# Optimization experiments

Measured on AMD Instinct MI355X. Metric: run time of the kernel, lower is better.

The kernel has to match this reference:

```python
import jax, jax.numpy as jnp
import numpy as np

MI, DIS, DIN, HID, L, H, NG, H1, OUT = 2048, 1024, 3072, 256, 15, 8, 8, 512, 64
DENOM = 4.0 / 7.0  # (grid_max - grid_min) / (num_grids - 1)
EPS = 1e-5


def _ln(x, g, b):
    m = jnp.mean(x, axis=-1, keepdims=True)
    v = jnp.mean((x - m) ** 2, axis=-1, keepdims=True)
    return (x - m) * jax.lax.rsqrt(v + EPS) * g + b


def _fastkan(x, ln_g, ln_b, grid, Ws, Wb, bb):
    xn = _ln(x, ln_g, ln_b)
    basis = jnp.exp(-(((xn[..., None] - grid) / DENOM) ** 2))  # [N, DIN, NG]
    ret = basis.reshape(x.shape[0], -1) @ Ws.T                  # SplineLinear (no bias)
    return ret + jax.nn.silu(x) @ Wb.T + bb                      # base update


def _hgcn(x, G, W, attn, bias, rW1, rb1, rW2, rb2, ln_g, ln_b, jk_W, jk_b):
    # per-layer multi-head conv: mean_h a_h * G @ (x @ W_h) == G @ (x @ (sum_h a_h W_h / H))
    def step(xc, p):
        W_l, a_l, b_l, rW1_l, rb1_l, rW2_l, rb2_l, g_l, be_l = p
        W_eff = jnp.einsum('h,hio->io', a_l, W_l) / H
        out = G @ (xc @ W_eff) + b_l
        gate = jax.nn.sigmoid(jax.nn.relu(out @ rW1_l.T + rb1_l) @ rW2_l.T + rb2_l)
        out = _ln(out * gate, g_l, be_l)
        out = jnp.where(out >= 0, out, 0.25 * out)  # leaky_relu(0.25); dropout off (eval)
        return out, out
    _, outs = jax.lax.scan(step, x, (W, attn, bias, rW1, rb1, rW2, rb2, ln_g, ln_b))
    jk = jnp.moveaxis(outs, 0, 1).reshape(x.shape[0], L * HID)   # jumping-knowledge concat
    return jk @ jk_W.T + jk_b


def _mlp3(x, W1, b1, W2, b2, W3, b3):
    h = jax.nn.relu(x @ W1.T + b1)
    h = jax.nn.relu(h @ W2.T + b2)
    return jax.nn.relu(h @ W3.T + b3)


def _forward(concat_mi, concat_dis, G_mi, G_dis, AT, A, rbf_grid, mi_kan_ln_g, mi_kan_ln_b, mi_kan_Ws, mi_kan_Wb, mi_kan_bb, dis_kan_ln_g, dis_kan_ln_b, dis_kan_Ws, dis_kan_Wb, dis_kan_bb, mi_W, mi_attn, mi_bias, mi_rW1, mi_rb1, mi_rW2, mi_rb2, mi_ln_g, mi_ln_b, mi_jk_W, mi_jk_b, dis_W, dis_attn, dis_bias, dis_rW1, dis_rb1, dis_rW2, dis_rb2, dis_ln_g, dis_ln_b, dis_jk_W, dis_jk_b, lx_W1, lx_b1, lx_W2, lx_b2, lx_W3, lx_b3, ly_W1, ly_b1, ly_W2, ly_b2, ly_W3, ly_b3, ne_W, ne_b, he_W, he_b, mun_W, mun_b, mue_W, mue_b):
    # AT and A are accepted by the original forward but never used in its body.
    mi_e = _fastkan(concat_mi, mi_kan_ln_g, mi_kan_ln_b, rbf_grid, mi_kan_Ws, mi_kan_Wb, mi_kan_bb)
    dis_e = _fastkan(concat_dis, dis_kan_ln_g, dis_kan_ln_b, rbf_grid, dis_kan_Ws, dis_kan_Wb, dis_kan_bb)
    mi_f = _hgcn(mi_e, G_mi, mi_W, mi_attn, mi_bias, mi_rW1, mi_rb1, mi_rW2, mi_rb2, mi_ln_g, mi_ln_b, mi_jk_W, mi_jk_b)
    dis_f = _hgcn(dis_e, G_dis, dis_W, dis_attn, dis_bias, dis_rW1, dis_rb1, dis_rW2, dis_rb2, dis_ln_g, dis_ln_b, dis_jk_W, dis_jk_b)
    x = _mlp3(mi_f, lx_W1, lx_b1, lx_W2, lx_b2, lx_W3, lx_b3)
    y = _mlp3(dis_f, ly_W1, ly_b1, ly_W2, ly_b2, ly_W3, ly_b3)
    result_h = x @ y.T                                           # [MI, DIS]
    z_node = jax.nn.relu(concat_mi @ ne_W.T + ne_b)              # node_encoders1 (eval: no dropout)
    z_edge = jax.nn.relu(concat_dis @ he_W.T + he_b)             # hyperedge_encoders1
    z_node_mean = z_node @ mun_W.T + mun_b                       # _enc_mu_node (identity act)
    z_edge_mean = z_edge @ mue_W.T + mue_b                       # _enc_mu_hedge
    recon = z_node_mean @ z_edge_mean.T                          # decoder2 with identity act
    score = 0.7 * jax.nn.sigmoid(recon) + 0.3 * jax.nn.sigmoid(result_h)
    return score, recon


def setup_inputs() -> dict:
    ks = iter(jax.random.split(jax.random.key(0), 96))
    nrm = lambda shape, s: jax.random.normal(next(ks), shape, dtype=jnp.float32) * s
    uni = lambda shape: jax.random.uniform(next(ks), shape, dtype=jnp.float32)
    d = {}
    d['concat_mi'] = nrm((MI, DIN), 1.0)
    d['concat_dis'] = nrm((DIS, DIN), 1.0)
    d['G_mi'] = uni((MI, MI)) / MI    # row-normalized dense hypergraph adjacency
    d['G_dis'] = uni((DIS, DIS)) / DIS
    d['AT'] = uni((DIS, MI))
    d['A'] = uni((MI, DIS))
    d['rbf_grid'] = jnp.linspace(-2.0, 2.0, NG).astype(jnp.float32)
    for p in ('mi', 'dis'):
        d[p + '_kan_ln_g'] = jnp.ones((DIN,), jnp.float32)
        d[p + '_kan_ln_b'] = jnp.zeros((DIN,), jnp.float32)
        d[p + '_kan_Ws'] = nrm((HID, DIN * NG), 0.02)
        d[p + '_kan_Wb'] = nrm((HID, DIN), 0.02)
        d[p + '_kan_bb'] = nrm((HID,), 0.01)
        d[p + '_W'] = nrm((L, H, HID, HID), 0.06)
        d[p + '_attn'] = jnp.ones((L, H), jnp.float32)
        d[p + '_bias'] = nrm((L, HID), 0.01)
        d[p + '_rW1'] = nrm((L, HID // 4, HID), 0.05)
        d[p + '_rb1'] = nrm((L, HID // 4), 0.01)
        d[p + '_rW2'] = nrm((L, HID, HID // 4), 0.05)
        d[p + '_rb2'] = nrm((L, HID), 0.01)
        d[p + '_ln_g'] = jnp.ones((L, HID), jnp.float32)
        d[p + '_ln_b'] = jnp.zeros((L, HID), jnp.float32)
        d[p + '_jk_W'] = nrm((HID, L * HID), 0.02)
        d[p + '_jk_b'] = nrm((HID,), 0.01)
    for p in ('lx', 'ly'):
        d[p + '_W1'] = nrm((256, HID), 0.05); d[p + '_b1'] = nrm((256,), 0.01)
        d[p + '_W2'] = nrm((128, 256), 0.05); d[p + '_b2'] = nrm((128,), 0.01)
        d[p + '_W3'] = nrm((64, 128), 0.05); d[p + '_b3'] = nrm((64,), 0.01)
    d['ne_W'] = nrm((H1, DIN), 0.02); d['ne_b'] = nrm((H1,), 0.01)
    d['he_W'] = nrm((H1, DIN), 0.02); d['he_b'] = nrm((H1,), 0.01)
    d['mun_W'] = nrm((OUT, H1), 0.02); d['mun_b'] = nrm((OUT,), 0.01)
    d['mue_W'] = nrm((OUT, H1), 0.02); d['mue_b'] = nrm((OUT,), 0.01)
    return d


def reference(concat_mi, concat_dis, G_mi, G_dis, AT, A, rbf_grid, mi_kan_ln_g, mi_kan_ln_b, mi_kan_Ws, mi_kan_Wb, mi_kan_bb, dis_kan_ln_g, dis_kan_ln_b, dis_kan_Ws, dis_kan_Wb, dis_kan_bb, mi_W, mi_attn, mi_bias, mi_rW1, mi_rb1, mi_rW2, mi_rb2, mi_ln_g, mi_ln_b, mi_jk_W, mi_jk_b, dis_W, dis_attn, dis_bias, dis_rW1, dis_rb1, dis_rW2, dis_rb2, dis_ln_g, dis_ln_b, dis_jk_W, dis_jk_b, lx_W1, lx_b1, lx_W2, lx_b2, lx_W3, lx_b3, ly_W1, ly_b1, ly_W2, ly_b2, ly_W3, ly_b3, ne_W, ne_b, he_W, he_b, mun_W, mun_b, mue_W, mue_b):
    return _forward(concat_mi, concat_dis, G_mi, G_dis, AT, A, rbf_grid, mi_kan_ln_g, mi_kan_ln_b, mi_kan_Ws, mi_kan_Wb, mi_kan_bb, dis_kan_ln_g, dis_kan_ln_b, dis_kan_Ws, dis_kan_Wb, dis_kan_bb, mi_W, mi_attn, mi_bias, mi_rW1, mi_rb1, mi_rW2, mi_rb2, mi_ln_g, mi_ln_b, mi_jk_W, mi_jk_b, dis_W, dis_attn, dis_bias, dis_rW1, dis_rb1, dis_rW2, dis_rb2, dis_ln_g, dis_ln_b, dis_jk_W, dis_jk_b, lx_W1, lx_b1, lx_W2, lx_b2, lx_W3, lx_b3, ly_W1, ly_b1, ly_W2, ly_b2, ly_W3, ly_b3, ne_W, ne_b, he_W, he_b, mun_W, mun_b, mue_W, mue_b)
```

## Files before the change

kernel.cpp:

```cpp
#include <hip/hip_runtime.h>
#include <cstdint>
#include <cstddef>

typedef unsigned short u16;
typedef __attribute__((ext_vector_type(8))) short short8;
typedef __attribute__((ext_vector_type(4))) float f32x4;

#define MI_N  2048
#define DIS_N 1024
#define TOT_N 3072
#define DIN   3072
#define HID   256
#define LL    15
#define NG    8

__device__ __forceinline__ float b2f(u16 u) {
  unsigned int v = ((unsigned int)u) << 16;
  float f;
  __builtin_memcpy(&f, &v, 4);
  return f;
}
__device__ __forceinline__ u16 f2b(float f) {
  unsigned int u;
  __builtin_memcpy(&u, &f, 4);
  u = (u + 0x7fffu + ((u >> 16) & 1u)) >> 16;
  return (u16)u;
}
__device__ __forceinline__ float sigf(float x) { return 1.f / (1.f + __expf(-x)); }

#define NSEG 20
struct CvtJobs {
  const float* src[NSEG];
  u16* dst[NSEG];
  int nblk[NSEG];
  int nseg;
};

__global__ __launch_bounds__(256) void cvt_f2b(CvtJobs j) {
  int b = blockIdx.x, s = 0;
  while (s + 1 < j.nseg && b >= j.nblk[s]) { b -= j.nblk[s]; ++s; }
  const long base = ((long)b * 256 + threadIdx.x) * 8;
  const float4 v0 = *(const float4*)(j.src[s] + base);
  const float4 v1 = *(const float4*)(j.src[s] + base + 4);
  short8 o;
  o[0] = (short)f2b(v0.x); o[1] = (short)f2b(v0.y);
  o[2] = (short)f2b(v0.z); o[3] = (short)f2b(v0.w);
  o[4] = (short)f2b(v1.x); o[5] = (short)f2b(v1.y);
  o[6] = (short)f2b(v1.z); o[7] = (short)f2b(v1.w);
  *(short8*)(j.dst[s] + base) = o;
}

struct GP {
  const u16* A; int lda;
  const u16* B; int ldb;
  void* C; int ldc;
  const float* bias;
  int K;
  int mblk;
};

template <int ACT, int TRANS, int F32OUT, int NCT>
__global__ __launch_bounds__(64) void gemm_bt(GP p0, GP p1) {
  GP p = p0;
  int bx = blockIdx.x;
  if (bx >= p0.mblk) { bx -= p0.mblk; p = p1; }
  const int lane = threadIdx.x;
  const int m16 = lane & 15, quad = lane >> 4;
  const int kph = quad * 8;
  const long row0 = (long)bx * 32 + m16;
  const long colBase = (long)blockIdx.y * (16 * NCT);
  f32x4 acc[2][NCT] = {};
  const u16* A0 = p.A + row0 * (long)p.lda + kph;
  const u16* A1 = A0 + 16L * p.lda;
  const u16* Bb = p.B + (colBase + m16) * (long)p.ldb + kph;
  const long bstep = 16L * p.ldb;
  for (int kk = 0; kk < p.K; kk += 32) {
    short8 a0 = *(const short8*)(A0 + kk);
    short8 a1 = *(const short8*)(A1 + kk);
#pragma unroll
    for (int c = 0; c < NCT; ++c) {
      short8 b = *(const short8*)(Bb + c * bstep + kk);
      acc[0][c] = __builtin_amdgcn_mfma_f32_16x16x32_bf16(a0, b, acc[0][c], 0, 0, 0);
      acc[1][c] = __builtin_amdgcn_mfma_f32_16x16x32_bf16(a1, b, acc[1][c], 0, 0, 0);
    }
  }
#pragma unroll
  for (int c = 0; c < NCT; ++c) {
    const long col = colBase + c * 16 + m16;
    const float bv = p.bias ? p.bias[col] : 0.f;
#pragma unroll
    for (int r = 0; r < 2; ++r) {
      const long orow = (long)bx * 32 + r * 16 + quad * 4;
#pragma unroll
      for (int j = 0; j < 4; ++j) {
        float v = acc[r][c][j] + bv;
        if (ACT == 1) v = fmaxf(v, 0.f);
        if (ACT == 2) v = sigf(v);
        if (F32OUT)
          ((float*)p.C)[(orow + j) * (long)p.ldc + col] = v;
        else if (TRANS)
          ((u16*)p.C)[col * (long)p.ldc + orow + j] = f2b(v);
        else
          ((u16*)p.C)[(orow + j) * (long)p.ldc + col] = f2b(v);
      }
    }
  }
}

struct FKP {
  const u16* xn; const u16* xb;
  const u16* Ws; const u16* Wb;
  float* partial;
  int rowoff;
  int mblk;
};

__global__ __launch_bounds__(64) void fastkan_gemm(FKP p0, FKP p1, const float* grid8) {
  FKP p = p0;
  int bx = blockIdx.x;
  if (bx >= p0.mblk) { bx -= p0.mblk; p = p1; }
  const int chunk = blockIdx.z;
  const int lane = threadIdx.x;
  const int m16 = lane & 15, quad = lane >> 4, kph = quad * 8;
  const long row0 = (long)bx * 32 + m16;
  const long colBase = (long)blockIdx.y * 128;
  f32x4 acc[2][8] = {};
  if (chunk < 4) {
    float gv[8];
#pragma unroll
    for (int j = 0; j < 8; ++j) gv[j] = grid8[j];
    const u16* xn0 = p.xn + row0 * (long)DIN;
    const u16* xn1 = xn0 + 16L * DIN;
    const int k0 = chunk * 6144, k1 = k0 + 6144;
    for (int kk = k0; kk < k1; kk += 32) {
      const int d = (kk >> 3) + quad;
      const float x0 = b2f(xn0[d]);
      const float x1 = b2f(xn1[d]);
      short8 a0, a1;
#pragma unroll
      for (int j = 0; j < 8; ++j) {
        float t0 = (x0 - gv[j]) * 1.75f;
        float t1 = (x1 - gv[j]) * 1.75f;
        a0[j] = (short)f2b(__expf(-t0 * t0));
        a1[j] = (short)f2b(__expf(-t1 * t1));
      }
#pragma unroll
      for (int c = 0; c < 8; ++c) {
        const u16* Bp = p.Ws + (colBase + c * 16 + m16) * (long)(DIN * NG) + kk + kph;
        short8 b = *(const short8*)Bp;
        acc[0][c] = __builtin_amdgcn_mfma_f32_16x16x32_bf16(a0, b, acc[0][c], 0, 0, 0);
        acc[1][c] = __builtin_amdgcn_mfma_f32_16x16x32_bf16(a1, b, acc[1][c], 0, 0, 0);
      }
    }
  } else {
    const u16* x0p = p.xb + row0 * (long)DIN + kph;
    const u16* x1p = x0p + 16L * DIN;
    for (int kk = 0; kk < DIN; kk += 32) {
      short8 r0 = *(const short8*)(x0p + kk);
      short8 r1 = *(const short8*)(x1p + kk);
      short8 a0, a1;
#pragma unroll
      for (int j = 0; j < 8; ++j) {
        float v0 = b2f((u16)r0[j]);
        float v1 = b2f((u16)r1[j]);
        a0[j] = (short)f2b(v0 * sigf(v0));
        a1[j] = (short)f2b(v1 * sigf(v1));
      }
#pragma unroll
      for (int c = 0; c < 8; ++c) {
        const u16* Bp = p.Wb + (colBase + c * 16 + m16) * (long)DIN + kk + kph;
        short8 b = *(const short8*)Bp;
        acc[0][c] = __builtin_amdgcn_mfma_f32_16x16x32_bf16(a0, b, acc[0][c], 0, 0, 0);
        acc[1][c] = __builtin_amdgcn_mfma_f32_16x16x32_bf16(a1, b, acc[1][c], 0, 0, 0);
      }
    }
  }
  float* outp = p.partial + ((long)chunk * TOT_N + p.rowoff) * HID;
#pragma unroll
  for (int c = 0; c < 8; ++c) {
    const long col = colBase + c * 16 + m16;
#pragma unroll
    for (int r = 0; r < 2; ++r) {
      const long orow = (long)bx * 32 + r * 16 + quad * 4;
#pragma unroll
      for (int j = 0; j < 4; ++j) outp[(orow + j) * HID + col] = acc[r][c][j];
    }
  }
}

__global__ __launch_bounds__(256) void fk_combine(const float* partial, const float* bb_mi,
                                                  const float* bb_dis, u16* e) {
  const long i = (long)blockIdx.x * 256 + threadIdx.x;
  const int c = (int)(i & 255);
  const long n = i >> 8;
  float s = 0.f;
#pragma unroll
  for (int pI = 0; pI < 5; ++pI) s += partial[(long)pI * TOT_N * HID + i];
  s += (n < MI_N ? bb_mi : bb_dis)[c];
  e[i] = f2b(s);
}

__global__ __launch_bounds__(256) void weff_kernel(const float* Wmi, const float* Ami,
                                                   const float* Wdis, const float* Adis,
                                                   u16* outT) {
  const int b = blockIdx.x;
  const int s = b / 3840;
  const int r = b % 3840;
  const int l = r >> 8;
  const int t = r & 255;
  const int i0 = (t >> 4) << 4;
  const int o0 = (t & 15) << 4;
  const float* W = (s ? Wdis : Wmi) + (long)l * 8 * 65536;
  const float* A = (s ? Adis : Ami) + l * 8;
  const int tx = threadIdx.x & 15;
  const int ty = threadIdx.x >> 4;
  float sum = 0.f;
#pragma unroll
  for (int h = 0; h < 8; ++h)
    sum += A[h] * W[(long)h * 65536 + (long)(i0 + ty) * 256 + o0 + tx];
  sum *= 0.125f;
  __shared__ float tile[16][17];
  tile[ty][tx] = sum;
  __syncthreads();
  outT[((long)s * LL + l) * 65536 + (long)(o0 + ty) * 256 + i0 + tx] = f2b(tile[tx][ty]);
}

__device__ __forceinline__ void breduce2(float& a, float& b) {
  for (int o = 32; o > 0; o >>= 1) {
    a += __shfl_down(a, o);
    b += __shfl_down(b, o);
  }
  __shared__ float sm[8];
  const int w = threadIdx.x >> 6;
  const int lane = threadIdx.x & 63;
  if (lane == 0) { sm[w] = a; sm[4 + w] = b; }
  __syncthreads();
  if (threadIdx.x == 0) {
    sm[0] = sm[0] + sm[1] + sm[2] + sm[3];
    sm[4] = sm[4] + sm[5] + sm[6] + sm[7];
  }
  __syncthreads();
  a = sm[0];
  b = sm[4];
}

__global__ __launch_bounds__(256) void ln_silu(const float* xmi, const float* xdis,
                                               const float* gmi, const float* bmi,
                                               const float* gdis, const float* bdis,
                                               u16* xn, u16* cbf) {
  const int n = blockIdx.x;
  const bool ds = (n >= MI_N);
  const float* x = ds ? xdis + (long)(n - MI_N) * DIN : xmi + (long)n * DIN;
  const float* g = ds ? gdis : gmi;
  const float* be = ds ? bdis : bmi;
  float xv[12];
  float s1 = 0.f, s2 = 0.f;
#pragma unroll
  for (int j = 0; j < 12; ++j) {
    xv[j] = x[j * 256 + threadIdx.x];
    s1 += xv[j];
    s2 += xv[j] * xv[j];
  }
  breduce2(s1, s2);
  const float m = s1 * (1.f / DIN);
  const float inv = rsqrtf(s2 * (1.f / DIN) - m * m + 1e-5f);
#pragma unroll
  for (int j = 0; j < 12; ++j) {
    const int e = j * 256 + threadIdx.x;
    xn[(long)n * DIN + e] = f2b((xv[j] - m) * inv * g[e] + be[e]);
    cbf[(long)n * DIN + e] = f2b(xv[j]);
  }
}

__global__ __launch_bounds__(256) void gate_ln(const u16* hout, const u16* gate,
                                               const float* gmi, const float* bmi,
                                               const float* gdis, const float* bdis,
                                               u16* jk, int l) {
  const int n = blockIdx.x;
  const int c = threadIdx.x;
  const bool ds = (n >= MI_N);
  const float* g = (ds ? gdis : gmi) + l * HID;
  const float* be = (ds ? bdis : bmi) + l * HID;
  const float h = b2f(hout[(long)n * HID + c]) * b2f(gate[(long)n * HID + c]);
  float s1 = h, s2 = h * h;
  breduce2(s1, s2);
  const float m = s1 * (1.f / HID);
  const float var = s2 * (1.f / HID) - m * m;
  float y = (h - m) * rsqrtf(var + 1e-5f) * g[c] + be[c];
  y = (y >= 0.f) ? y : 0.25f * y;
  jk[(long)n * (LL * HID) + l * HID + c] = f2b(y);
}

__global__ __launch_bounds__(256) void final_combine(const float* rh, float* out) {
  const long i = (long)blockIdx.x * 256 + threadIdx.x;
  const float rc = out[(long)MI_N * DIS_N + i];
  out[i] = 0.7f * sigf(rc) + 0.3f * sigf(rh[i]);
}

extern "C" void kernel_launch(void* const* d_in, const int* in_sizes, int n_in,
                              void* d_out, int out_size, void* d_ws, size_t ws_size,
                              hipStream_t stream) {
  const float* concat_mi   = (const float*)d_in[0];
  const float* concat_dis  = (const float*)d_in[1];
  const float* G_mi        = (const float*)d_in[2];
  const float* G_dis       = (const float*)d_in[3];
  const float* rbf_grid    = (const float*)d_in[6];
  const float* mi_kan_ln_g = (const float*)d_in[7];
  const float* mi_kan_ln_b = (const float*)d_in[8];
  const float* mi_kan_Ws   = (const float*)d_in[9];
  const float* mi_kan_Wb   = (const float*)d_in[10];
  const float* mi_kan_bb   = (const float*)d_in[11];
  const float* mi_W        = (const float*)d_in[12];
  const float* mi_attn     = (const float*)d_in[13];
  const float* mi_bias     = (const float*)d_in[14];
  const float* mi_rW1      = (const float*)d_in[15];
  const float* mi_rb1      = (const float*)d_in[16];
  const float* mi_rW2      = (const float*)d_in[17];
  const float* mi_rb2      = (const float*)d_in[18];
  const float* mi_ln_g     = (const float*)d_in[19];
  const float* mi_ln_b     = (const float*)d_in[20];
  const float* mi_jk_W     = (const float*)d_in[21];
  const float* mi_jk_b     = (const float*)d_in[22];
  const float* dis_kan_ln_g = (const float*)d_in[23];
  const float* dis_kan_ln_b = (const float*)d_in[24];
  const float* dis_kan_Ws  = (const float*)d_in[25];
  const float* dis_kan_Wb  = (const float*)d_in[26];
  const float* dis_kan_bb  = (const float*)d_in[27];
  const float* dis_W       = (const float*)d_in[28];
  const float* dis_attn    = (const float*)d_in[29];
  const float* dis_bias    = (const float*)d_in[30];
  const float* dis_rW1     = (const float*)d_in[31];
  const float* dis_rb1     = (const float*)d_in[32];
  const float* dis_rW2     = (const float*)d_in[33];
  const float* dis_rb2     = (const float*)d_in[34];
  const float* dis_ln_g    = (const float*)d_in[35];
  const float* dis_ln_b    = (const float*)d_in[36];
  const float* dis_jk_W    = (const float*)d_in[37];
  const float* dis_jk_b    = (const float*)d_in[38];
  const float* lx_W1 = (const float*)d_in[39]; const float* lx_b1 = (const float*)d_in[40];
  const float* lx_W2 = (const float*)d_in[41]; const float* lx_b2 = (const float*)d_in[42];
  const float* lx_W3 = (const float*)d_in[43]; const float* lx_b3 = (const float*)d_in[44];
  const float* ly_W1 = (const float*)d_in[45]; const float* ly_b1 = (const float*)d_in[46];
  const float* ly_W2 = (const float*)d_in[47]; const float* ly_b2 = (const float*)d_in[48];
  const float* ly_W3 = (const float*)d_in[49]; const float* ly_b3 = (const float*)d_in[50];
  const float* ne_W  = (const float*)d_in[51]; const float* ne_b  = (const float*)d_in[52];
  const float* he_W  = (const float*)d_in[53]; const float* he_b  = (const float*)d_in[54];
  const float* mun_W = (const float*)d_in[55]; const float* mun_b = (const float*)d_in[56];
  const float* mue_W = (const float*)d_in[57]; const float* mue_b = (const float*)d_in[58];

  char* wp = (char*)d_ws;
  size_t off = 0;
  auto alloc = [&](size_t bytes) -> void* {
    void* p = wp + off;
    off += (bytes + 255) & ~(size_t)255;
    return p;
  };
  u16* cbf    = (u16*)alloc((size_t)TOT_N * DIN * 2);
  u16* gmib   = (u16*)alloc((size_t)MI_N * MI_N * 2);
  u16* gdisb  = (u16*)alloc((size_t)DIS_N * DIS_N * 2);
  u16* wsb0   = (u16*)alloc((size_t)256 * 24576 * 2);
  u16* wsb1   = (u16*)alloc((size_t)256 * 24576 * 2);
  u16* wbb0   = (u16*)alloc((size_t)256 * 3072 * 2);
  u16* wbb1   = (u16*)alloc((size_t)256 * 3072 * 2);
  u16* jkwb0  = (u16*)alloc((size_t)256 * 3840 * 2);
  u16* jkwb1  = (u16*)alloc((size_t)256 * 3840 * 2);
  u16* rw1b0  = (u16*)alloc((size_t)LL * 64 * 256 * 2);
  u16* rw1b1  = (u16*)alloc((size_t)LL * 64 * 256 * 2);
  u16* rw2b0  = (u16*)alloc((size_t)LL * 256 * 64 * 2);
  u16* rw2b1  = (u16*)alloc((size_t)LL * 256 * 64 * 2);
  u16* lxw1b  = (u16*)alloc((size_t)256 * 256 * 2);
  u16* lxw2b  = (u16*)alloc((size_t)128 * 256 * 2);
  u16* lxw3b  = (u16*)alloc((size_t)64 * 128 * 2);
  u16* lyw1b  = (u16*)alloc((size_t)256 * 256 * 2);
  u16* lyw2b  = (u16*)alloc((size_t)128 * 256 * 2);
  u16* lyw3b  = (u16*)alloc((size_t)64 * 128 * 2);
  u16* neb    = (u16*)alloc((size_t)512 * 3072 * 2);
  u16* heb    = (u16*)alloc((size_t)512 * 3072 * 2);
  u16* munb   = (u16*)alloc((size_t)64 * 512 * 2);
  u16* mueb   = (u16*)alloc((size_t)64 * 512 * 2);
  u16* wefft  = (u16*)alloc((size_t)2 * LL * 65536 * 2);
  u16* e      = (u16*)alloc((size_t)TOT_N * HID * 2);
  u16* t1t    = (u16*)alloc((size_t)HID * TOT_N * 2);
  u16* hout   = (u16*)alloc((size_t)TOT_N * HID * 2);
  u16* g1b    = (u16*)alloc((size_t)TOT_N * 64 * 2);
  u16* gateb  = (u16*)alloc((size_t)TOT_N * HID * 2);
  u16* jk     = (u16*)alloc((size_t)TOT_N * LL * HID * 2);
  u16* fb     = (u16*)alloc((size_t)TOT_N * HID * 2);
  char* regA  = (char*)alloc(35000000);
  u16* xn     = (u16*)regA;
  float* fkp  = (float*)(regA + 18874624);
  u16* h1b    = (u16*)regA;
  u16* h2b    = (u16*)(regA + 1572864);
  u16* xyb    = (u16*)(regA + 2359296);
  float* rh   = (float*)(regA + 2752512);
  u16* zb     = (u16*)(regA + 11141120);
  u16* zm     = (u16*)(regA + 14286848);
  float* outf = (float*)d_out;
  float* rec  = outf + (size_t)MI_N * DIS_N;
  (void)ws_size; (void)in_sizes; (void)n_in; (void)out_size;

  const dim3 B64(64), B256(256);

  {
    CvtJobs cj{};
    int ns = 0, total = 0;
    auto push = [&](const float* s, u16* dst, int count) {
      cj.src[ns] = s; cj.dst[ns] = dst; cj.nblk[ns] = count / 2048;
      total += count / 2048; ++ns;
    };
    push(G_mi, gmib, MI_N * MI_N);
    push(G_dis, gdisb, DIS_N * DIS_N);
    push(mi_kan_Ws, wsb0, 256 * 24576);
    push(dis_kan_Ws, wsb1, 256 * 24576);
    push(mi_kan_Wb, wbb0, 256 * 3072);
    push(dis_kan_Wb, wbb1, 256 * 3072);
    push(mi_jk_W, jkwb0, 256 * 3840);
    push(dis_jk_W, jkwb1, 256 * 3840);
    push(mi_rW1, rw1b0, LL * 64 * 256);
    push(dis_rW1, rw1b1, LL * 64 * 256);
    push(mi_rW2, rw2b0, LL * 256 * 64);
    push(dis_rW2, rw2b1, LL * 256 * 64);
    push(lx_W1, lxw1b, 256 * 256);
    push(lx_W2, lxw2b, 128 * 256);
    push(lx_W3, lxw3b, 64 * 128);
    push(ly_W1, lyw1b, 256 * 256);
    push(ly_W2, lyw2b, 128 * 256);
    push(ly_W3, lyw3b, 64 * 128);
    push(ne_W, neb, 512 * 3072);
    push(he_W, heb, 512 * 3072);
    cj.nseg = ns;
    cvt_f2b<<<dim3(total), B256, 0, stream>>>(cj);
    CvtJobs cj2{};
    cj2.src[0] = mun_W; cj2.dst[0] = munb; cj2.nblk[0] = (64 * 512) / 2048;
    cj2.src[1] = mue_W; cj2.dst[1] = mueb; cj2.nblk[1] = (64 * 512) / 2048;
    cj2.nseg = 2;
    cvt_f2b<<<dim3(32), B256, 0, stream>>>(cj2);
  }
  ln_silu<<<dim3(TOT_N), B256, 0, stream>>>(concat_mi, concat_dis, mi_kan_ln_g, mi_kan_ln_b,
                                            dis_kan_ln_g, dis_kan_ln_b, xn, cbf);
  weff_kernel<<<dim3(2 * LL * 256), B256, 0, stream>>>(mi_W, mi_attn, dis_W, dis_attn, wefft);
  {
    FKP f0{xn, cbf, wsb0, wbb0, fkp, 0, 64};
    FKP f1{xn + (size_t)MI_N * DIN, cbf + (size_t)MI_N * DIN, wsb1, wbb1, fkp, MI_N, 32};
    fastkan_gemm<<<dim3(96, 2, 5), B64, 0, stream>>>(f0, f1, rbf_grid);
    fk_combine<<<dim3(TOT_N * HID / 256), B256, 0, stream>>>(fkp, mi_kan_bb, dis_kan_bb, e);
  }
  for (int l = 0; l < LL; ++l) {
    const u16* xc0 = (l == 0) ? e : jk + (size_t)(l - 1) * HID;
    const u16* xc1 = (l == 0) ? e + (size_t)MI_N * HID
                              : jk + (size_t)MI_N * LL * HID + (size_t)(l - 1) * HID;
    const int xlda = (l == 0) ? HID : LL * HID;
    GP a0{xc0, xlda, wefft + (size_t)l * 65536, 256, t1t, MI_N, nullptr, 256, 64};
    GP a1{xc1, xlda, wefft + ((size_t)LL + l) * 65536, 256, t1t + (size_t)HID * MI_N, DIS_N,
          nullptr, 256, 32};
    gemm_bt<0, 1, 0, 4><<<dim3(96, 4), B64, 0, stream>>>(a0, a1);
    GP h0{gmib, MI_N, t1t, MI_N, hout, HID, mi_bias + l * HID, MI_N, 64};
    GP h1{gdisb, DIS_N, t1t + (size_t)HID * MI_N, DIS_N, hout + (size_t)MI_N * HID, HID,
          dis_bias + l * HID, DIS_N, 32};
    gemm_bt<0, 0, 0, 4><<<dim3(96, 4), B64, 0, stream>>>(h0, h1);
    GP g0{hout, HID, rw1b0 + (size_t)l * 64 * HID, HID, g1b, 64, mi_rb1 + l * 64, HID, 64};
    GP g1{hout + (size_t)MI_N * HID, HID, rw1b1 + (size_t)l * 64 * HID, HID,
          g1b + (size_t)MI_N * 64, 64, dis_rb1 + l * 64, HID, 32};
    gemm_bt<1, 0, 0, 4><<<dim3(96, 1), B64, 0, stream>>>(g0, g1);
    GP s0{g1b, 64, rw2b0 + (size_t)l * HID * 64, 64, gateb, HID, mi_rb2 + l * HID, 64, 64};
    GP s1{g1b + (size_t)MI_N * 64, 64, rw2b1 + (size_t)l * HID * 64, 64,
          gateb + (size_t)MI_N * HID, HID, dis_rb2 + l * HID, 64, 32};
    gemm_bt<2, 0, 0, 4><<<dim3(96, 4), B64, 0, stream>>>(s0, s1);
    gate_ln<<<dim3(TOT_N), B256, 0, stream>>>(hout, gateb, mi_ln_g, mi_ln_b, dis_ln_g,
                                              dis_ln_b, jk, l);
  }
  {
    GP j0{jk, LL * HID, jkwb0, LL * HID, fb, HID, mi_jk_b, LL * HID, 64};
    GP j1{jk + (size_t)MI_N * LL * HID, LL * HID, jkwb1, LL * HID, fb + (size_t)MI_N * HID,
          HID, dis_jk_b, LL * HID, 32};
    gemm_bt<0, 0, 0, 4><<<dim3(96, 4), B64, 0, stream>>>(j0, j1);
  }
  {
    GP m0{fb, HID, lxw1b, HID, h1b, 256, lx_b1, HID, 64};
    GP m1{fb + (size_t)MI_N * HID, HID, lyw1b, HID, h1b + (size_t)MI_N * 256, 256, ly_b1,
          HID, 32};
    gemm_bt<1, 0, 0, 4><<<dim3(96, 4), B64, 0, stream>>>(m0, m1);
    GP n0{h1b, 256, lxw2b, 256, h2b, 128, lx_b2, 256, 64};
    GP n1{h1b + (size_t)MI_N * 256, 256, lyw2b, 256, h2b + (size_t)MI_N * 128, 128, ly_b2,
          256, 32};
    gemm_bt<1, 0, 0, 4><<<dim3(96, 2), B64, 0, stream>>>(n0, n1);
    GP o0{h2b, 128, lxw3b, 128, xyb, 64, lx_b3, 128, 64};
    GP o1{h2b + (size_t)MI_N * 128, 128, lyw3b, 128, xyb + (size_t)MI_N * 64, 64, ly_b3,
          128, 32};
    gemm_bt<1, 0, 0, 4><<<dim3(96, 1), B64, 0, stream>>>(o0, o1);
  }
  {
    GP r0{xyb, 64, xyb + (size_t)MI_N * 64, 64, rh, DIS_N, nullptr, 64, 64};
    gemm_bt<0, 0, 1, 4><<<dim3(64, 16), B64, 0, stream>>>(r0, r0);
  }
  {
    GP e0{cbf, DIN, neb, DIN, zb, 512, ne_b, DIN, 64};
    GP e1{cbf + (size_t)MI_N * DIN, DIN, heb, DIN, zb + (size_t)MI_N * 512, 512, he_b, DIN,
          32};
    gemm_bt<1, 0, 0, 4><<<dim3(96, 8), B64, 0, stream>>>(e0, e1);
  }
  {
    GP u0{zb, 512, munb, 512, zm, 64, mun_b, 512, 64};
    GP u1{zb + (size_t)MI_N * 512, 512, mueb, 512, zm + (size_t)MI_N * 64, 64, mue_b, 512,
          32};
    gemm_bt<0, 0, 0, 4><<<dim3(96, 1), B64, 0, stream>>>(u0, u1);
  }
  {
    GP c0{zm, 64, zm + (size_t)MI_N * 64, 64, rec, DIS_N, nullptr, 64, 64};
    gemm_bt<0, 0, 1, 4><<<dim3(64, 16), B64, 0, stream>>>(c0, c0);
  }
  final_combine<<<dim3(MI_N * DIS_N / 256), B256, 0, stream>>>(rh, outf);
}
```

Before: 1.690 ms.

## Split GEMM K-loop across four waves with LDS reduction

Both the generic GEMM kernel and the fastkan GEMM now launch 256 threads (four wavefronts) per block instead of 64. Each wave handles every fourth 32-wide K slice, and the partial accumulators are combined through shared memory in a two-step tree before wave 0 writes the result. The aim is more waves in flight on the small grids (96x4 blocks), which should better hide memory latency. In exchange it adds LDS traffic, barriers and register pressure. For small K (64) two waves get no slices and only contribute zeros.

```diff
diff --git a/kernel.cpp b/kernel.cpp
--- a/kernel.cpp
+++ b/kernel.cpp
@@ -60,11 +60,13 @@
 };
 
 template <int ACT, int TRANS, int F32OUT, int NCT>
-__global__ __launch_bounds__(64) void gemm_bt(GP p0, GP p1) {
+__global__ __launch_bounds__(256) void gemm_bt(GP p0, GP p1) {
   GP p = p0;
   int bx = blockIdx.x;
   if (bx >= p0.mblk) { bx -= p0.mblk; p = p1; }
-  const int lane = threadIdx.x;
+  const int tid = threadIdx.x;
+  const int w = tid >> 6;
+  const int lane = tid & 63;
   const int m16 = lane & 15, quad = lane >> 4;
   const int kph = quad * 8;
   const long row0 = (long)bx * 32 + m16;
@@ -74,7 +76,7 @@
   const u16* A1 = A0 + 16L * p.lda;
   const u16* Bb = p.B + (colBase + m16) * (long)p.ldb + kph;
   const long bstep = 16L * p.ldb;
-  for (int kk = 0; kk < p.K; kk += 32) {
+  for (int kk = w * 32; kk < p.K; kk += 128) {
     short8 a0 = *(const short8*)(A0 + kk);
     short8 a1 = *(const short8*)(A1 + kk);
 #pragma unroll
@@ -84,6 +86,26 @@
       acc[1][c] = __builtin_amdgcn_mfma_f32_16x16x32_bf16(a1, b, acc[1][c], 0, 0, 0);
     }
   }
+  __shared__ float red[2][64][NCT * 8 + 1];
+  float* av = (float*)acc;
+  if (w >= 2) {
+#pragma unroll
+    for (int i = 0; i < NCT * 8; ++i) red[w - 2][lane][i] = av[i];
+  }
+  __syncthreads();
+  if (w < 2) {
+#pragma unroll
+    for (int i = 0; i < NCT * 8; ++i) av[i] += red[w][lane][i];
+  }
+  __syncthreads();
+  if (w == 1) {
+#pragma unroll
+    for (int i = 0; i < NCT * 8; ++i) red[0][lane][i] = av[i];
+  }
+  __syncthreads();
+  if (w != 0) return;
+#pragma unroll
+  for (int i = 0; i < NCT * 8; ++i) av[i] += red[0][lane][i];
 #pragma unroll
   for (int c = 0; c < NCT; ++c) {
     const long col = colBase + c * 16 + m16;
@@ -115,12 +137,14 @@
   int mblk;
 };
 
-__global__ __launch_bounds__(64) void fastkan_gemm(FKP p0, FKP p1, const float* grid8) {
+__global__ __launch_bounds__(256) void fastkan_gemm(FKP p0, FKP p1, const float* grid8) {
   FKP p = p0;
   int bx = blockIdx.x;
   if (bx >= p0.mblk) { bx -= p0.mblk; p = p1; }
   const int chunk = blockIdx.z;
-  const int lane = threadIdx.x;
+  const int tid = threadIdx.x;
+  const int w = tid >> 6;
+  const int lane = tid & 63;
   const int m16 = lane & 15, quad = lane >> 4, kph = quad * 8;
   const long row0 = (long)bx * 32 + m16;
   const long colBase = (long)blockIdx.y * 128;
@@ -132,7 +156,7 @@
     const u16* xn0 = p.xn + row0 * (long)DIN;
     const u16* xn1 = xn0 + 16L * DIN;
     const int k0 = chunk * 6144, k1 = k0 + 6144;
-    for (int kk = k0; kk < k1; kk += 32) {
+    for (int kk = k0 + w * 32; kk < k1; kk += 128) {
       const int d = (kk >> 3) + quad;
       const float x0 = b2f(xn0[d]);
       const float x1 = b2f(xn1[d]);
@@ -155,7 +179,7 @@
   } else {
     const u16* x0p = p.xb + row0 * (long)DIN + kph;
     const u16* x1p = x0p + 16L * DIN;
-    for (int kk = 0; kk < DIN; kk += 32) {
+    for (int kk = w * 32; kk < DIN; kk += 128) {
       short8 r0 = *(const short8*)(x0p + kk);
       short8 r1 = *(const short8*)(x1p + kk);
       short8 a0, a1;
@@ -175,6 +199,26 @@
       }
     }
   }
+  __shared__ float red[2][64][65];
+  float* av = (float*)acc;
+  if (w >= 2) {
+#pragma unroll
+    for (int i = 0; i < 64; ++i) red[w - 2][lane][i] = av[i];
+  }
+  __syncthreads();
+  if (w < 2) {
+#pragma unroll
+    for (int i = 0; i < 64; ++i) av[i] += red[w][lane][i];
+  }
+  __syncthreads();
+  if (w == 1) {
+#pragma unroll
+    for (int i = 0; i < 64; ++i) red[0][lane][i] = av[i];
+  }
+  __syncthreads();
+  if (w != 0) return;
+#pragma unroll
+  for (int i = 0; i < 64; ++i) av[i] += red[0][lane][i];
   float* outp = p.partial + ((long)chunk * TOT_N + p.rowoff) * HID;
 #pragma unroll
   for (int c = 0; c < 8; ++c) {
@@ -399,7 +443,7 @@
   float* rec  = outf + (size_t)MI_N * DIS_N;
   (void)ws_size; (void)in_sizes; (void)n_in; (void)out_size;
 
-  const dim3 B64(64), B256(256);
+  const dim3 B256(256);
 
   {
     CvtJobs cj{};
@@ -442,7 +486,7 @@
   {
     FKP f0{xn, cbf, wsb0, wbb0, fkp, 0, 64};
     FKP f1{xn + (size_t)MI_N * DIN, cbf + (size_t)MI_N * DIN, wsb1, wbb1, fkp, MI_N, 32};
-    fastkan_gemm<<<dim3(96, 2, 5), B64, 0, stream>>>(f0, f1, rbf_grid);
+    fastkan_gemm<<<dim3(96, 2, 5), B256, 0, stream>>>(f0, f1, rbf_grid);
     fk_combine<<<dim3(TOT_N * HID / 256), B256, 0, stream>>>(fkp, mi_kan_bb, dis_kan_bb, e);
   }
   for (int l = 0; l < LL; ++l) {
@@ -453,19 +497,19 @@
     GP a0{xc0, xlda, wefft + (size_t)l * 65536, 256, t1t, MI_N, nullptr, 256, 64};
     GP a1{xc1, xlda, wefft + ((size_t)LL + l) * 65536, 256, t1t + (size_t)HID * MI_N, DIS_N,
           nullptr, 256, 32};
-    gemm_bt<0, 1, 0, 4><<<dim3(96, 4), B64, 0, stream>>>(a0, a1);
+    gemm_bt<0, 1, 0, 4><<<dim3(96, 4), B256, 0, stream>>>(a0, a1);
     GP h0{gmib, MI_N, t1t, MI_N, hout, HID, mi_bias + l * HID, MI_N, 64};
     GP h1{gdisb, DIS_N, t1t + (size_t)HID * MI_N, DIS_N, hout + (size_t)MI_N * HID, HID,
           dis_bias + l * HID, DIS_N, 32};
-    gemm_bt<0, 0, 0, 4><<<dim3(96, 4), B64, 0, stream>>>(h0, h1);
+    gemm_bt<0, 0, 0, 4><<<dim3(96, 4), B256, 0, stream>>>(h0, h1);
     GP g0{hout, HID, rw1b0 + (size_t)l * 64 * HID, HID, g1b, 64, mi_rb1 + l * 64, HID, 64};
     GP g1{hout + (size_t)MI_N * HID, HID, rw1b1 + (size_t)l * 64 * HID, HID,
           g1b + (size_t)MI_N * 64, 64, dis_rb1 + l * 64, HID, 32};
-    gemm_bt<1, 0, 0, 4><<<dim3(96, 1), B64, 0, stream>>>(g0, g1);
+    gemm_bt<1, 0, 0, 4><<<dim3(96, 1), B256, 0, stream>>>(g0, g1);
     GP s0{g1b, 64, rw2b0 + (size_t)l * HID * 64, 64, gateb, HID, mi_rb2 + l * HID, 64, 64};
     GP s1{g1b + (size_t)MI_N * 64, 64, rw2b1 + (size_t)l * HID * 64, 64,
           gateb + (size_t)MI_N * HID, HID, dis_rb2 + l * HID, 64, 32};
-    gemm_bt<2, 0, 0, 4><<<dim3(96, 4), B64, 0, stream>>>(s0, s1);
+    gemm_bt<2, 0, 0, 4><<<dim3(96, 4), B256, 0, stream>>>(s0, s1);
     gate_ln<<<dim3(TOT_N), B256, 0, stream>>>(hout, gateb, mi_ln_g, mi_ln_b, dis_ln_g,
                                               dis_ln_b, jk, l);
   }
@@ -473,41 +517,41 @@
     GP j0{jk, LL * HID, jkwb0, LL * HID, fb, HID, mi_jk_b, LL * HID, 64};
     GP j1{jk + (size_t)MI_N * LL * HID, LL * HID, jkwb1, LL * HID, fb + (size_t)MI_N * HID,
           HID, dis_jk_b, LL * HID, 32};
-    gemm_bt<0, 0, 0, 4><<<dim3(96, 4), B64, 0, stream>>>(j0, j1);
+    gemm_bt<0, 0, 0, 4><<<dim3(96, 4), B256, 0, stream>>>(j0, j1);
   }
   {
     GP m0{fb, HID, lxw1b, HID, h1b, 256, lx_b1, HID, 64};
     GP m1{fb + (size_t)MI_N * HID, HID, lyw1b, HID, h1b + (size_t)MI_N * 256, 256, ly_b1,
           HID, 32};
-    gemm_bt<1, 0, 0, 4><<<dim3(96, 4), B64, 0, stream>>>(m0, m1);
+    gemm_bt<1, 0, 0, 4><<<dim3(96, 4), B256, 0, stream>>>(m0, m1);
     GP n0{h1b, 256, lxw2b, 256, h2b, 128, lx_b2, 256, 64};
     GP n1{h1b + (size_t)MI_N * 256, 256, lyw2b, 256, h2b + (size_t)MI_N * 128, 128, ly_b2,
           256, 32};
-    gemm_bt<1, 0, 0, 4><<<dim3(96, 2), B64, 0, stream>>>(n0, n1);
+    gemm_bt<1, 0, 0, 4><<<dim3(96, 2), B256, 0, stream>>>(n0, n1);
     GP o0{h2b, 128, lxw3b, 128, xyb, 64, lx_b3, 128, 64};
     GP o1{h2b + (size_t)MI_N * 128, 128, lyw3b, 128, xyb + (size_t)MI_N * 64, 64, ly_b3,
           128, 32};
-    gemm_bt<1, 0, 0, 4><<<dim3(96, 1), B64, 0, stream>>>(o0, o1);
+    gemm_bt<1, 0, 0, 4><<<dim3(96, 1), B256, 0, stream>>>(o0, o1);
   }
   {
     GP r0{xyb, 64, xyb + (size_t)MI_N * 64, 64, rh, DIS_N, nullptr, 64, 64};
-    gemm_bt<0, 0, 1, 4><<<dim3(64, 16), B64, 0, stream>>>(r0, r0);
+    gemm_bt<0, 0, 1, 4><<<dim3(64, 16), B256, 0, stream>>>(r0, r0);
   }
   {
     GP e0{cbf, DIN, neb, DIN, zb, 512, ne_b, DIN, 64};
     GP e1{cbf + (size_t)MI_N * DIN, DIN, heb, DIN, zb + (size_t)MI_N * 512, 512, he_b, DIN,
           32};
-    gemm_bt<1, 0, 0, 4><<<dim3(96, 8), B64, 0, stream>>>(e0, e1);
+    gemm_bt<1, 0, 0, 4><<<dim3(96, 8), B256, 0, stream>>>(e0, e1);
   }
   {
     GP u0{zb, 512, munb, 512, zm, 64, mun_b, 512, 64};
     GP u1{zb + (size_t)MI_N * 512, 512, mueb, 512, zm + (size_t)MI_N * 64, 64, mue_b, 512,
           32};
-    gemm_bt<0, 0, 0, 4><<<dim3(96, 1), B64, 0, stream>>>(u0, u1);
+    gemm_bt<0, 0, 0, 4><<<dim3(96, 1), B256, 0, stream>>>(u0, u1);
   }
   {
     GP c0{zm, 64, zm + (size_t)MI_N * 64, 64, rec, DIS_N, nullptr, 64, 64};
-    gemm_bt<0, 0, 1, 4><<<dim3(64, 16), B64, 0, stream>>>(c0, c0);
+    gemm_bt<0, 0, 1, 4><<<dim3(64, 16), B256, 0, stream>>>(c0, c0);
   }
   final_combine<<<dim3(MI_N * DIS_N / 256), B256, 0, stream>>>(rh, outf);
 }
```

Result: faster. 1.458 ms (-13.7%).
